# Optimization experiments

Hardware: AMD Instinct MI355X
Metric: run time of the kernel (lower is better)

## Reference

```python
import jax, jax.numpy as jnp
import numpy as np

B, T, H, I, O, R = 64, 1024, 1024, 8, 8, 4
NOISE_STD, ALPHA = 0.05, 0.2


def setup_inputs() -> dict:
    key = jax.random.key(0)
    ks = jax.random.split(key, 6)
    return {
        "x": jax.random.normal(ks[0], (B, T, I), jnp.float32),
        "noise": jax.random.normal(ks[1], (B, T, H), jnp.float32),
        "wi": jax.random.normal(ks[2], (I, H), jnp.float32),
        "si": jnp.ones((I,), jnp.float32),
        "m": jax.random.normal(ks[3], (H, R), jnp.float32),
        "n": jax.random.normal(ks[4], (H, R), jnp.float32),
        "b": jnp.zeros((H,), jnp.float32),
        "wo": jax.random.normal(ks[5], (H, O), jnp.float32) / H,
        "so": jnp.ones((O,), jnp.float32),
        "h0": jnp.zeros((H,), jnp.float32),
    }


def reference(x, noise, wi, si, m, n, b, wo, so, h0):
    hidden = h0.shape[0]
    batch = x.shape[0]
    wi_full = wi * si[:, None]          # (I, H): (wi.T * si).T
    wo_full = wo * so                   # (H, O)
    h_init = jnp.broadcast_to(h0, (batch, hidden))
    r_init = jnp.tanh(h_init)           # non_linearity(initial_states)
    # precompute input drive for all steps: (B,T,H) -> scan over time-major
    u = jnp.einsum('bti,ih->tbh', x, wi_full)
    noise_t = jnp.transpose(noise, (1, 0, 2))  # (T,B,H)

    def step(carry, inp):
        h, r = carry
        u_i, nz_i = inp
        rec = (r @ n) @ m.T / hidden                    # low-rank recurrence
        h = h + NOISE_STD * nz_i + ALPHA * (-h + rec + u_i)
        r = jnp.tanh(h + b)
        out = h @ wo_full                               # identity output nonlin
        return (h, r), out

    _, outs = jax.lax.scan(step, (h_init, r_init), (u, noise_t))
    return jnp.transpose(outs, (1, 0, 2))  # (B,T,O)
```

## Files before the change

### kernel.cpp

```cpp
#include <hip/hip_runtime.h>

#define BB 64
#define TT 1024
#define HH 1024
#define II 8
#define OO 8
#define RRK 4
#define NOISE_STD 0.05f
#define ALPHA 0.2f

typedef float v4f __attribute__((ext_vector_type(4)));
typedef float v2f __attribute__((ext_vector_type(2)));

#define C2E 2.885390081777927f

template<int CTRL, int RM>
__device__ __forceinline__ float dpp_add(float acc, float src) {
    int s = __builtin_amdgcn_update_dpp(0, __float_as_int(src), CTRL, RM, 0xF, true);
    return acc + __int_as_float(s);
}

__device__ __forceinline__ float wave_sum(float x) {
    x = dpp_add<0xB1, 0xF>(x, x);
    x = dpp_add<0x4E, 0xF>(x, x);
    x = dpp_add<0x141, 0xF>(x, x);
    x = dpp_add<0x140, 0xF>(x, x);
    x = dpp_add<0x142, 0xA>(x, x);
    x = dpp_add<0x143, 0xC>(x, x);
    return x;
}

__device__ __forceinline__ float tanh_from_l2x(float l2x) {
    float e = __builtin_amdgcn_exp2f(l2x);
    float r = __builtin_amdgcn_rcpf(e + 1.0f);
    return fmaf(-2.0f, r, 1.0f);
}

__device__ __forceinline__ void block_sync_lds() {
    asm volatile("s_waitcnt lgkmcnt(0)\n\ts_barrier" ::: "memory");
}

__global__ __launch_bounds__(256)
void prew_kernel(const float* __restrict__ noise, const float* __restrict__ wo,
                 const float* __restrict__ so, float* __restrict__ W) {
    __shared__ __align__(16) float red[2][8][4][8];

    const int tid  = threadIdx.x;
    const int wave = tid >> 6;
    const int lane = tid & 63;
    const int e0   = tid << 2;

    float woa[4][OO];
    {
        float so8[OO];
        #pragma unroll
        for (int o = 0; o < OO; ++o) so8[o] = so[o] * NOISE_STD;
        #pragma unroll
        for (int e = 0; e < 4; ++e) {
            const float4 a4 = *(const float4*)(wo + (e0 + e) * OO);
            const float4 b4 = *(const float4*)(wo + (e0 + e) * OO + 4);
            woa[e][0] = a4.x * so8[0]; woa[e][1] = a4.y * so8[1];
            woa[e][2] = a4.z * so8[2]; woa[e][3] = a4.w * so8[3];
            woa[e][4] = b4.x * so8[4]; woa[e][5] = b4.y * so8[5];
            woa[e][6] = b4.z * so8[6]; woa[e][7] = b4.w * so8[7];
        }
    }

    const int row0 = blockIdx.x * 32;
    float4 nz[8], nzn[8];
    #pragma unroll
    for (int j = 0; j < 8; ++j)
        nz[j] = *(const float4*)(noise + (size_t)(row0 + j) * HH + e0);

    #pragma unroll
    for (int ph = 0; ph < 4; ++ph) {
        const int cur   = ph & 1;
        const int rbase = row0 + ph * 8;

        if (ph < 3) {
            #pragma unroll
            for (int j = 0; j < 8; ++j)
                nzn[j] = *(const float4*)(noise + (size_t)(rbase + 8 + j) * HH + e0);
        }

        #pragma unroll
        for (int j = 0; j < 8; ++j) {
            float op[OO];
            #pragma unroll
            for (int o = 0; o < OO; ++o)
                op[o] = fmaf(nz[j].x, woa[0][o], fmaf(nz[j].y, woa[1][o],
                        fmaf(nz[j].z, woa[2][o], nz[j].w * woa[3][o])));
            #pragma unroll
            for (int o = 0; o < OO; ++o) op[o] = wave_sum(op[o]);
            if (lane == 63) {
                *(float4*)&red[cur][j][wave][0] = make_float4(op[0], op[1], op[2], op[3]);
                *(float4*)&red[cur][j][wave][4] = make_float4(op[4], op[5], op[6], op[7]);
            }
        }
        block_sync_lds();
        if (tid < 64) {
            const int j = tid >> 3, o = tid & 7;
            W[(rbase + j) * OO + o] = (red[cur][j][0][o] + red[cur][j][1][o]) +
                                      (red[cur][j][2][o] + red[cur][j][3][o]);
        }
        #pragma unroll
        for (int j = 0; j < 8; ++j) nz[j] = nzn[j];
    }
}

__global__ __launch_bounds__(512, 1)
void rnn_seq_kernel(const float* __restrict__ x, const float* __restrict__ noise,
                    const float* __restrict__ wi, const float* __restrict__ si,
                    const float* __restrict__ mM, const float* __restrict__ nM,
                    const float* __restrict__ bv, const float* __restrict__ wo,
                    const float* __restrict__ so, const float* __restrict__ h0,
                    const float* __restrict__ W, float* __restrict__ out) {
    __shared__ __align__(16) float lds_x[(TT + 1) * II];
    __shared__ __align__(16) float lds_W[TT * OO];
    __shared__ __align__(16) float lds_out[TT * OO];
    __shared__ __align__(16) float red[4][8][4];
    __shared__ __align__(16) float redc[8][104];
    __shared__ float ambx[104];

    const int tid  = threadIdx.x;
    const int b    = blockIdx.x;
    const int wave = tid >> 6;
    const int lane = tid & 63;
    const int e0   = tid << 1;
    const int oc   = tid & 7;

    {
        const float4* sx = (const float4*)(x + (size_t)b * (TT * II));
        const float4* sw = (const float4*)(W + (size_t)b * (TT * OO));
        float4* dx = (float4*)lds_x;
        float4* dw = (float4*)lds_W;
        #pragma unroll
        for (int k = 0; k < 4; ++k) {
            dx[k * 512 + tid] = sx[k * 512 + tid];
            dw[k * 512 + tid] = sw[k * 512 + tid];
        }
        if (tid < 2) dx[2048 + tid] = sx[2046 + tid];
    }

    v2f wiac[II];
    #pragma unroll
    for (int i = 0; i < II; ++i) {
        const float s  = ALPHA * si[i];
        const v2f w = *(const v2f*)(wi + i * HH + e0);
        wiac[i] = s * w;
    }
    v4f nr0, nr1;
    v4f ma0, ma1;
    v2f mac[RRK];
    {
        const float cs = ALPHA / (float)HH;
        ma0 = cs * *(const v4f*)(mM + (size_t)e0 * RRK);
        ma1 = cs * *(const v4f*)(mM + (size_t)(e0 + 1) * RRK);
        nr0 = *(const v4f*)(nM + (size_t)e0 * RRK);
        nr1 = *(const v4f*)(nM + (size_t)(e0 + 1) * RRK);
        mac[0] = (v2f){ma0.x, ma1.x};
        mac[1] = (v2f){ma0.y, ma1.y};
        mac[2] = (v2f){ma0.z, ma1.z};
        mac[3] = (v2f){ma0.w, ma1.w};
    }
    float woa[2][OO];
    {
        #pragma unroll
        for (int e = 0; e < 2; ++e) {
            const float4 a4 = *(const float4*)(wo + (e0 + e) * OO);
            const float4 b4 = *(const float4*)(wo + (e0 + e) * OO + 4);
            woa[e][0] = a4.x * so[0]; woa[e][1] = a4.y * so[1];
            woa[e][2] = a4.z * so[2]; woa[e][3] = a4.w * so[3];
            woa[e][4] = b4.x * so[4]; woa[e][5] = b4.y * so[5];
            woa[e][6] = b4.z * so[6]; woa[e][7] = b4.w * so[7];
        }
    }
    v2f tb2e, h, r;
    {
        const v2f b2 = *(const v2f*)(bv + e0);
        tb2e = C2E * b2;
        h = *(const v2f*)(h0 + e0);
        v2f targ = C2E * h;
        r.x = tanh_from_l2x(targ.x);
        r.y = tanh_from_l2x(targ.y);
    }

    #pragma unroll
    for (int kg = 0; kg < 26; ++kg) {
        float p[4];
        #pragma unroll
        for (int u = 0; u < 4; ++u) {
            const int k = kg * 4 + u;
            float s;
            if (k < 32) {
                const int q = k >> 3, o = k & 7;
                const float m0 = (q == 0) ? ma0.x : (q == 1) ? ma0.y : (q == 2) ? ma0.z : ma0.w;
                const float m1 = (q == 0) ? ma1.x : (q == 1) ? ma1.y : (q == 2) ? ma1.z : ma1.w;
                s = fmaf(m0, woa[0][o], m1 * woa[1][o]);
            } else if (k < 96) {
                const int i = (k - 32) >> 3, o = k & 7;
                s = fmaf(wiac[i].x, woa[0][o], wiac[i].y * woa[1][o]);
            } else {
                const int o = k - 96;
                s = fmaf(h.x, woa[0][o], h.y * woa[1][o]);
            }
            p[u] = wave_sum(s);
        }
        if (lane == 63)
            *(float4*)&redc[wave][kg * 4] = make_float4(p[0], p[1], p[2], p[3]);
    }
    block_sync_lds();
    if (tid < 104)
        ambx[tid] = ((redc[0][tid] + redc[1][tid]) + (redc[2][tid] + redc[3][tid])) +
                    ((redc[4][tid] + redc[5][tid]) + (redc[6][tid] + redc[7][tid]));
    __syncthreads();

    float Amr[RRK], Bxr[II], y;
    #pragma unroll
    for (int q = 0; q < RRK; ++q) Amr[q] = ambx[q * 8 + oc];
    #pragma unroll
    for (int i = 0; i < II; ++i) Bxr[i] = ambx[32 + i * 8 + oc];
    y = ambx[96 + oc];

    const float* nzp = noise + (size_t)b * (TT * HH) + e0;
    v2f nzb[4];
    #pragma unroll
    for (int j = 0; j < 4; ++j) nzb[j] = *(const v2f*)(nzp + j * HH);

    v4f xqc0 = *(const v4f*)&lds_x[0];
    v4f xqc1 = *(const v4f*)&lds_x[4];
    float wqc = lds_W[oc];

    for (int t0 = 0; t0 < TT; t0 += 4) {
        #pragma unroll
        for (int j = 0; j < 4; ++j) {
            const int t = t0 + j;

            const int tn = t + 1;
            const v4f xqn0 = *(const v4f*)&lds_x[tn * II];
            const v4f xqn1 = *(const v4f*)&lds_x[tn * II + 4];
            const float wqn = lds_W[(tn & (TT - 1)) * OO + oc];

            v4f vpv = r.x * nr0;
            vpv += r.y * nr1;
            float vp0 = wave_sum(vpv.x);
            float vp1 = wave_sum(vpv.y);
            float vp2 = wave_sum(vpv.z);
            float vp3 = wave_sum(vpv.w);
            if (lane == 63)
                *(float4*)&red[j][wave][0] = make_float4(vp0, vp1, vp2, vp3);

            float ybase = fmaf(xqc0.x, Bxr[0], wqc);
            ybase = fmaf(xqc0.y, Bxr[1], ybase);
            ybase = fmaf(xqc0.z, Bxr[2], ybase);
            ybase = fmaf(xqc0.w, Bxr[3], ybase);
            ybase = fmaf(xqc1.x, Bxr[4], ybase);
            ybase = fmaf(xqc1.y, Bxr[5], ybase);
            ybase = fmaf(xqc1.z, Bxr[6], ybase);
            ybase = fmaf(xqc1.w, Bxr[7], ybase);

            v2f auv = xqc0.x * wiac[0];
            auv += xqc0.y * wiac[1];
            auv += xqc0.z * wiac[2];
            auv += xqc0.w * wiac[3];
            auv += xqc1.x * wiac[4];
            auv += xqc1.y * wiac[5];
            auv += xqc1.z * wiac[6];
            auv += xqc1.w * wiac[7];

            block_sync_lds();

            v4f vs;
            {
                const v4f s0 = *(const v4f*)&red[j][0][0];
                const v4f s1 = *(const v4f*)&red[j][1][0];
                const v4f s2 = *(const v4f*)&red[j][2][0];
                const v4f s3 = *(const v4f*)&red[j][3][0];
                const v4f s4 = *(const v4f*)&red[j][4][0];
                const v4f s5 = *(const v4f*)&red[j][5][0];
                const v4f s6 = *(const v4f*)&red[j][6][0];
                const v4f s7 = *(const v4f*)&red[j][7][0];
                vs = ((s0 + s1) + (s2 + s3)) + ((s4 + s5) + (s6 + s7));
            }

            v2f acc = auv;
            acc += vs.x * mac[0];
            acc += vs.y * mac[1];
            acc += vs.z * mac[2];
            acc += vs.w * mac[3];
            h = (1.0f - ALPHA) * h + acc;
            h += NOISE_STD * nzb[j];

            {
                float t4 = fmaf(vs.x, Amr[0], ybase);
                t4 = fmaf(vs.y, Amr[1], t4);
                t4 = fmaf(vs.z, Amr[2], t4);
                t4 = fmaf(vs.w, Amr[3], t4);
                y = fmaf(1.0f - ALPHA, y, t4);
                if (tid < OO) lds_out[t * OO + tid] = y;
            }

            nzb[j] = *(const v2f*)(nzp + ((t + 4) & (TT - 1)) * HH);

            {
                v2f targ = C2E * h + tb2e;
                r.x = tanh_from_l2x(targ.x);
                r.y = tanh_from_l2x(targ.y);
            }

            xqc0 = xqn0; xqc1 = xqn1; wqc = wqn;
        }
    }

    __syncthreads();
    {
        float4* dst = (float4*)(out + (size_t)b * (TT * OO));
        const float4* srcv = (const float4*)lds_out;
        #pragma unroll
        for (int k = 0; k < 4; ++k)
            dst[k * 512 + tid] = srcv[k * 512 + tid];
    }
}

extern "C" void kernel_launch(void* const* d_in, const int* in_sizes, int n_in,
                              void* d_out, int out_size, void* d_ws, size_t ws_size,
                              hipStream_t stream) {
    const float* x     = (const float*)d_in[0];
    const float* noise = (const float*)d_in[1];
    const float* wi    = (const float*)d_in[2];
    const float* si    = (const float*)d_in[3];
    const float* mM    = (const float*)d_in[4];
    const float* nM    = (const float*)d_in[5];
    const float* bv    = (const float*)d_in[6];
    const float* wo    = (const float*)d_in[7];
    const float* so    = (const float*)d_in[8];
    const float* h0    = (const float*)d_in[9];
    float* out = (float*)d_out;
    float* W   = (float*)d_ws;

    prew_kernel<<<dim3(2048), dim3(256), 0, stream>>>(noise, wo, so, W);
    rnn_seq_kernel<<<dim3(BB), dim3(512), 0, stream>>>(
        x, noise, wi, si, mM, nM, bv, wo, so, h0, W, out);
}
```

Baseline: 924.8 us.

## Shrink RNN block to two waves and defer output via parallel chunked scan

The sequential RNN kernel now uses 128 threads with 8 hidden units per thread instead of 512 threads with 2. This cuts the cross-wave reduction to two partial sums per step, so each step's barrier involves fewer waves. The per-step output recurrence is removed from the serial loop. Only the rank-4 projection is stored per step, and outputs are rebuilt afterwards with a chunked linear scan (16 chunks of 64 steps, combined using the decay raised to the 64th power). The trade-off is more per-thread work and registers on the serial critical path, and far fewer waves to hide the noise-load latency.

```diff
diff --git a/kernel.cpp b/kernel.cpp
--- a/kernel.cpp
+++ b/kernel.cpp
@@ -10,7 +10,6 @@
 #define ALPHA 0.2f
 
 typedef float v4f __attribute__((ext_vector_type(4)));
-typedef float v2f __attribute__((ext_vector_type(2)));
 
 #define C2E 2.885390081777927f
 
@@ -108,7 +107,7 @@
     }
 }
 
-__global__ __launch_bounds__(512, 1)
+__global__ __launch_bounds__(128, 1)
 void rnn_seq_kernel(const float* __restrict__ x, const float* __restrict__ noise,
                     const float* __restrict__ wi, const float* __restrict__ si,
                     const float* __restrict__ mM, const float* __restrict__ nM,
@@ -116,73 +115,74 @@
                     const float* __restrict__ so, const float* __restrict__ h0,
                     const float* __restrict__ W, float* __restrict__ out) {
     __shared__ __align__(16) float lds_x[(TT + 1) * II];
-    __shared__ __align__(16) float lds_W[TT * OO];
+    __shared__ __align__(16) float lds_v[TT * RRK];
     __shared__ __align__(16) float lds_out[TT * OO];
-    __shared__ __align__(16) float red[4][8][4];
-    __shared__ __align__(16) float redc[8][104];
+    __shared__ __align__(16) float red[4][2][4];
+    __shared__ __align__(16) float redc[2][104];
     __shared__ float ambx[104];
+    __shared__ float chs[16][OO];
 
     const int tid  = threadIdx.x;
     const int b    = blockIdx.x;
     const int wave = tid >> 6;
     const int lane = tid & 63;
-    const int e0   = tid << 1;
+    const int e0   = tid << 3;
     const int oc   = tid & 7;
 
     {
         const float4* sx = (const float4*)(x + (size_t)b * (TT * II));
-        const float4* sw = (const float4*)(W + (size_t)b * (TT * OO));
         float4* dx = (float4*)lds_x;
-        float4* dw = (float4*)lds_W;
-        #pragma unroll
-        for (int k = 0; k < 4; ++k) {
-            dx[k * 512 + tid] = sx[k * 512 + tid];
-            dw[k * 512 + tid] = sw[k * 512 + tid];
-        }
+        #pragma unroll
+        for (int k = 0; k < 16; ++k)
+            dx[k * 128 + tid] = sx[k * 128 + tid];
         if (tid < 2) dx[2048 + tid] = sx[2046 + tid];
     }
 
-    v2f wiac[II];
+    v4f wiaA[II], wiaB[II];
     #pragma unroll
     for (int i = 0; i < II; ++i) {
-        const float s  = ALPHA * si[i];
-        const v2f w = *(const v2f*)(wi + i * HH + e0);
-        wiac[i] = s * w;
-    }
-    v4f nr0, nr1;
-    v4f ma0, ma1;
-    v2f mac[RRK];
+        const float s = ALPHA * si[i];
+        wiaA[i] = s * *(const v4f*)(wi + (size_t)i * HH + e0);
+        wiaB[i] = s * *(const v4f*)(wi + (size_t)i * HH + e0 + 4);
+    }
+    v4f nrv[8];
+    #pragma unroll
+    for (int e = 0; e < 8; ++e)
+        nrv[e] = *(const v4f*)(nM + (size_t)(e0 + e) * RRK);
+    v4f maA[RRK], maB[RRK];
     {
         const float cs = ALPHA / (float)HH;
-        ma0 = cs * *(const v4f*)(mM + (size_t)e0 * RRK);
-        ma1 = cs * *(const v4f*)(mM + (size_t)(e0 + 1) * RRK);
-        nr0 = *(const v4f*)(nM + (size_t)e0 * RRK);
-        nr1 = *(const v4f*)(nM + (size_t)(e0 + 1) * RRK);
-        mac[0] = (v2f){ma0.x, ma1.x};
-        mac[1] = (v2f){ma0.y, ma1.y};
-        mac[2] = (v2f){ma0.z, ma1.z};
-        mac[3] = (v2f){ma0.w, ma1.w};
-    }
-    float woa[2][OO];
-    {
-        #pragma unroll
-        for (int e = 0; e < 2; ++e) {
-            const float4 a4 = *(const float4*)(wo + (e0 + e) * OO);
-            const float4 b4 = *(const float4*)(wo + (e0 + e) * OO + 4);
-            woa[e][0] = a4.x * so[0]; woa[e][1] = a4.y * so[1];
-            woa[e][2] = a4.z * so[2]; woa[e][3] = a4.w * so[3];
-            woa[e][4] = b4.x * so[4]; woa[e][5] = b4.y * so[5];
-            woa[e][6] = b4.z * so[6]; woa[e][7] = b4.w * so[7];
-        }
-    }
-    v2f tb2e, h, r;
-    {
-        const v2f b2 = *(const v2f*)(bv + e0);
-        tb2e = C2E * b2;
-        h = *(const v2f*)(h0 + e0);
-        v2f targ = C2E * h;
-        r.x = tanh_from_l2x(targ.x);
-        r.y = tanh_from_l2x(targ.y);
+        v4f mrow[8];
+        #pragma unroll
+        for (int e = 0; e < 8; ++e)
+            mrow[e] = cs * *(const v4f*)(mM + (size_t)(e0 + e) * RRK);
+        #pragma unroll
+        for (int q = 0; q < RRK; ++q) {
+            maA[q] = (v4f){mrow[0][q], mrow[1][q], mrow[2][q], mrow[3][q]};
+            maB[q] = (v4f){mrow[4][q], mrow[5][q], mrow[6][q], mrow[7][q]};
+        }
+    }
+    float woa[8][OO];
+    #pragma unroll
+    for (int e = 0; e < 8; ++e) {
+        const float4 a4 = *(const float4*)(wo + (size_t)(e0 + e) * OO);
+        const float4 b4 = *(const float4*)(wo + (size_t)(e0 + e) * OO + 4);
+        woa[e][0] = a4.x * so[0]; woa[e][1] = a4.y * so[1];
+        woa[e][2] = a4.z * so[2]; woa[e][3] = a4.w * so[3];
+        woa[e][4] = b4.x * so[4]; woa[e][5] = b4.y * so[5];
+        woa[e][6] = b4.z * so[6]; woa[e][7] = b4.w * so[7];
+    }
+    v4f tbA, tbB, hA, hB, rA, rB;
+    {
+        tbA = C2E * *(const v4f*)(bv + e0);
+        tbB = C2E * *(const v4f*)(bv + e0 + 4);
+        hA = *(const v4f*)(h0 + e0);
+        hB = *(const v4f*)(h0 + e0 + 4);
+        const v4f ta = C2E * hA, tb = C2E * hB;
+        rA.x = tanh_from_l2x(ta.x); rA.y = tanh_from_l2x(ta.y);
+        rA.z = tanh_from_l2x(ta.z); rA.w = tanh_from_l2x(ta.w);
+        rB.x = tanh_from_l2x(tb.x); rB.y = tanh_from_l2x(tb.y);
+        rB.z = tanh_from_l2x(tb.z); rB.w = tanh_from_l2x(tb.w);
     }
 
     #pragma unroll
@@ -194,15 +194,34 @@
             float s;
             if (k < 32) {
                 const int q = k >> 3, o = k & 7;
-                const float m0 = (q == 0) ? ma0.x : (q == 1) ? ma0.y : (q == 2) ? ma0.z : ma0.w;
-                const float m1 = (q == 0) ? ma1.x : (q == 1) ? ma1.y : (q == 2) ? ma1.z : ma1.w;
-                s = fmaf(m0, woa[0][o], m1 * woa[1][o]);
+                s = maA[q].x * woa[0][o];
+                s = fmaf(maA[q].y, woa[1][o], s);
+                s = fmaf(maA[q].z, woa[2][o], s);
+                s = fmaf(maA[q].w, woa[3][o], s);
+                s = fmaf(maB[q].x, woa[4][o], s);
+                s = fmaf(maB[q].y, woa[5][o], s);
+                s = fmaf(maB[q].z, woa[6][o], s);
+                s = fmaf(maB[q].w, woa[7][o], s);
             } else if (k < 96) {
                 const int i = (k - 32) >> 3, o = k & 7;
-                s = fmaf(wiac[i].x, woa[0][o], wiac[i].y * woa[1][o]);
+                s = wiaA[i].x * woa[0][o];
+                s = fmaf(wiaA[i].y, woa[1][o], s);
+                s = fmaf(wiaA[i].z, woa[2][o], s);
+                s = fmaf(wiaA[i].w, woa[3][o], s);
+                s = fmaf(wiaB[i].x, woa[4][o], s);
+                s = fmaf(wiaB[i].y, woa[5][o], s);
+                s = fmaf(wiaB[i].z, woa[6][o], s);
+                s = fmaf(wiaB[i].w, woa[7][o], s);
             } else {
                 const int o = k - 96;
-                s = fmaf(h.x, woa[0][o], h.y * woa[1][o]);
+                s = hA.x * woa[0][o];
+                s = fmaf(hA.y, woa[1][o], s);
+                s = fmaf(hA.z, woa[2][o], s);
+                s = fmaf(hA.w, woa[3][o], s);
+                s = fmaf(hB.x, woa[4][o], s);
+                s = fmaf(hB.y, woa[5][o], s);
+                s = fmaf(hB.z, woa[6][o], s);
+                s = fmaf(hB.w, woa[7][o], s);
             }
             p[u] = wave_sum(s);
         }
@@ -211,114 +230,140 @@
     }
     block_sync_lds();
     if (tid < 104)
-        ambx[tid] = ((redc[0][tid] + redc[1][tid]) + (redc[2][tid] + redc[3][tid])) +
-                    ((redc[4][tid] + redc[5][tid]) + (redc[6][tid] + redc[7][tid]));
+        ambx[tid] = redc[0][tid] + redc[1][tid];
     __syncthreads();
 
-    float Amr[RRK], Bxr[II], y;
+    const float* nzp0 = noise + (size_t)b * (TT * HH) + e0;
+    v4f nzA[4], nzB[4];
+    #pragma unroll
+    for (int j = 0; j < 4; ++j) {
+        nzA[j] = *(const v4f*)(nzp0 + (size_t)j * HH);
+        nzB[j] = *(const v4f*)(nzp0 + (size_t)j * HH + 4);
+    }
+    const float* nzq = nzp0 + (size_t)4 * HH;
+
+    v4f xc0 = *(const v4f*)&lds_x[0];
+    v4f xc1 = *(const v4f*)&lds_x[4];
+
+#define RNN_STEP(t, j, PF)                                                     \
+    {                                                                          \
+        const v4f xn0 = *(const v4f*)&lds_x[((t) + 1) * II];                   \
+        const v4f xn1 = *(const v4f*)&lds_x[((t) + 1) * II + 4];               \
+        v4f vpa = rA.x * nrv[0];                                               \
+        v4f vpb = rB.x * nrv[4];                                               \
+        vpa += rA.y * nrv[1]; vpb += rB.y * nrv[5];                            \
+        vpa += rA.z * nrv[2]; vpb += rB.z * nrv[6];                            \
+        vpa += rA.w * nrv[3]; vpb += rB.w * nrv[7];                            \
+        const v4f vp = vpa + vpb;                                              \
+        const float vp0 = wave_sum(vp.x); const float vp1 = wave_sum(vp.y);    \
+        const float vp2 = wave_sum(vp.z); const float vp3 = wave_sum(vp.w);    \
+        if (lane == 63)                                                        \
+            *(float4*)&red[j][wave][0] = make_float4(vp0, vp1, vp2, vp3);      \
+        v4f auA = xc0.x * wiaA[0], auB = xc0.x * wiaB[0];                      \
+        auA += xc0.y * wiaA[1]; auB += xc0.y * wiaB[1];                        \
+        auA += xc0.z * wiaA[2]; auB += xc0.z * wiaB[2];                        \
+        auA += xc0.w * wiaA[3]; auB += xc0.w * wiaB[3];                        \
+        auA += xc1.x * wiaA[4]; auB += xc1.x * wiaB[4];                        \
+        auA += xc1.y * wiaA[5]; auB += xc1.y * wiaB[5];                        \
+        auA += xc1.z * wiaA[6]; auB += xc1.z * wiaB[6];                        \
+        auA += xc1.w * wiaA[7]; auB += xc1.w * wiaB[7];                        \
+        block_sync_lds();                                                      \
+        const v4f vs = *(const v4f*)&red[j][0][0] + *(const v4f*)&red[j][1][0];\
+        if (tid == 0) *(v4f*)&lds_v[(t) * RRK] = vs;                           \
+        v4f accA = auA + vs.x * maA[0], accB = auB + vs.x * maB[0];            \
+        accA += vs.y * maA[1]; accB += vs.y * maB[1];                          \
+        accA += vs.z * maA[2]; accB += vs.z * maB[2];                          \
+        accA += vs.w * maA[3]; accB += vs.w * maB[3];                          \
+        hA = (1.0f - ALPHA) * hA + accA;  hA += NOISE_STD * nzA[j];            \
+        hB = (1.0f - ALPHA) * hB + accB;  hB += NOISE_STD * nzB[j];            \
+        if (PF) {                                                              \
+            nzA[j] = *(const v4f*)nzq;                                         \
+            nzB[j] = *(const v4f*)(nzq + 4);                                   \
+            nzq += HH;                                                         \
+        }                                                                      \
+        const v4f tgA = C2E * hA + tbA, tgB = C2E * hB + tbB;                  \
+        rA.x = tanh_from_l2x(tgA.x); rA.y = tanh_from_l2x(tgA.y);              \
+        rA.z = tanh_from_l2x(tgA.z); rA.w = tanh_from_l2x(tgA.w);              \
+        rB.x = tanh_from_l2x(tgB.x); rB.y = tanh_from_l2x(tgB.y);              \
+        rB.z = tanh_from_l2x(tgB.z); rB.w = tanh_from_l2x(tgB.w);              \
+        xc0 = xn0; xc1 = xn1;                                                  \
+    }
+
+    for (int t0 = 0; t0 < TT - 4; t0 += 4) {
+        RNN_STEP(t0 + 0, 0, 1)
+        RNN_STEP(t0 + 1, 1, 1)
+        RNN_STEP(t0 + 2, 2, 1)
+        RNN_STEP(t0 + 3, 3, 1)
+    }
+    RNN_STEP(TT - 4, 0, 0)
+    RNN_STEP(TT - 3, 1, 0)
+    RNN_STEP(TT - 2, 2, 0)
+    RNN_STEP(TT - 1, 3, 0)
+#undef RNN_STEP
+
+    __syncthreads();
+
+    float Bxr[II], Amr[RRK];
     #pragma unroll
     for (int q = 0; q < RRK; ++q) Amr[q] = ambx[q * 8 + oc];
     #pragma unroll
     for (int i = 0; i < II; ++i) Bxr[i] = ambx[32 + i * 8 + oc];
-    y = ambx[96 + oc];
-
-    const float* nzp = noise + (size_t)b * (TT * HH) + e0;
-    v2f nzb[4];
-    #pragma unroll
-    for (int j = 0; j < 4; ++j) nzb[j] = *(const v2f*)(nzp + j * HH);
-
-    v4f xqc0 = *(const v4f*)&lds_x[0];
-    v4f xqc1 = *(const v4f*)&lds_x[4];
-    float wqc = lds_W[oc];
-
-    for (int t0 = 0; t0 < TT; t0 += 4) {
-        #pragma unroll
-        for (int j = 0; j < 4; ++j) {
-            const int t = t0 + j;
-
-            const int tn = t + 1;
-            const v4f xqn0 = *(const v4f*)&lds_x[tn * II];
-            const v4f xqn1 = *(const v4f*)&lds_x[tn * II + 4];
-            const float wqn = lds_W[(tn & (TT - 1)) * OO + oc];
-
-            v4f vpv = r.x * nr0;
-            vpv += r.y * nr1;
-            float vp0 = wave_sum(vpv.x);
-            float vp1 = wave_sum(vpv.y);
-            float vp2 = wave_sum(vpv.z);
-            float vp3 = wave_sum(vpv.w);
-            if (lane == 63)
-                *(float4*)&red[j][wave][0] = make_float4(vp0, vp1, vp2, vp3);
-
-            float ybase = fmaf(xqc0.x, Bxr[0], wqc);
-            ybase = fmaf(xqc0.y, Bxr[1], ybase);
-            ybase = fmaf(xqc0.z, Bxr[2], ybase);
-            ybase = fmaf(xqc0.w, Bxr[3], ybase);
-            ybase = fmaf(xqc1.x, Bxr[4], ybase);
-            ybase = fmaf(xqc1.y, Bxr[5], ybase);
-            ybase = fmaf(xqc1.z, Bxr[6], ybase);
-            ybase = fmaf(xqc1.w, Bxr[7], ybase);
-
-            v2f auv = xqc0.x * wiac[0];
-            auv += xqc0.y * wiac[1];
-            auv += xqc0.z * wiac[2];
-            auv += xqc0.w * wiac[3];
-            auv += xqc1.x * wiac[4];
-            auv += xqc1.y * wiac[5];
-            auv += xqc1.z * wiac[6];
-            auv += xqc1.w * wiac[7];
-
-            block_sync_lds();
-
-            v4f vs;
-            {
-                const v4f s0 = *(const v4f*)&red[j][0][0];
-                const v4f s1 = *(const v4f*)&red[j][1][0];
-                const v4f s2 = *(const v4f*)&red[j][2][0];
-                const v4f s3 = *(const v4f*)&red[j][3][0];
-                const v4f s4 = *(const v4f*)&red[j][4][0];
-                const v4f s5 = *(const v4f*)&red[j][5][0];
-                const v4f s6 = *(const v4f*)&red[j][6][0];
-                const v4f s7 = *(const v4f*)&red[j][7][0];
-                vs = ((s0 + s1) + (s2 + s3)) + ((s4 + s5) + (s6 + s7));
-            }
-
-            v2f acc = auv;
-            acc += vs.x * mac[0];
-            acc += vs.y * mac[1];
-            acc += vs.z * mac[2];
-            acc += vs.w * mac[3];
-            h = (1.0f - ALPHA) * h + acc;
-            h += NOISE_STD * nzb[j];
-
-            {
-                float t4 = fmaf(vs.x, Amr[0], ybase);
-                t4 = fmaf(vs.y, Amr[1], t4);
-                t4 = fmaf(vs.z, Amr[2], t4);
-                t4 = fmaf(vs.w, Amr[3], t4);
-                y = fmaf(1.0f - ALPHA, y, t4);
-                if (tid < OO) lds_out[t * OO + tid] = y;
-            }
-
-            nzb[j] = *(const v2f*)(nzp + ((t + 4) & (TT - 1)) * HH);
-
-            {
-                v2f targ = C2E * h + tb2e;
-                r.x = tanh_from_l2x(targ.x);
-                r.y = tanh_from_l2x(targ.y);
-            }
-
-            xqc0 = xqn0; xqc1 = xqn1; wqc = wqn;
-        }
-    }
-
+    const float y0v = ambx[96 + oc];
+
+    const int c   = tid >> 3;
+    const int t0c = c * 64;
+    float a64;
+    {
+        float a = 1.0f - ALPHA;
+        a = a * a; a = a * a; a = a * a;
+        a = a * a; a = a * a; a = a * a;
+        a64 = a;
+    }
+    const float* Wb = W + (size_t)b * (TT * OO);
+    float st[64];
+    float L = 0.0f;
+    #pragma unroll
+    for (int jt = 0; jt < 64; ++jt) {
+        const int t = t0c + jt;
+        const v4f xa = *(const v4f*)&lds_x[t * II];
+        const v4f xb = *(const v4f*)&lds_x[t * II + 4];
+        const v4f vv = *(const v4f*)&lds_v[t * RRK];
+        float s = Wb[t * OO + oc];
+        s = fmaf(xa.x, Bxr[0], s); s = fmaf(xa.y, Bxr[1], s);
+        s = fmaf(xa.z, Bxr[2], s); s = fmaf(xa.w, Bxr[3], s);
+        s = fmaf(xb.x, Bxr[4], s); s = fmaf(xb.y, Bxr[5], s);
+        s = fmaf(xb.z, Bxr[6], s); s = fmaf(xb.w, Bxr[7], s);
+        s = fmaf(vv.x, Amr[0], s); s = fmaf(vv.y, Amr[1], s);
+        s = fmaf(vv.z, Amr[2], s); s = fmaf(vv.w, Amr[3], s);
+        st[jt] = s;
+        L = fmaf(1.0f - ALPHA, L, s);
+    }
+    chs[c][oc] = L;
+    block_sync_lds();
+    if (tid < OO) {
+        float Y = ambx[96 + tid];
+        #pragma unroll
+        for (int c2 = 0; c2 < 16; ++c2) {
+            const float Lc = chs[c2][tid];
+            chs[c2][tid] = Y;
+            Y = fmaf(a64, Y, Lc);
+        }
+    }
+    block_sync_lds();
+    float yv = chs[c][oc];
+    (void)y0v;
+    #pragma unroll
+    for (int jt = 0; jt < 64; ++jt) {
+        yv = fmaf(1.0f - ALPHA, yv, st[jt]);
+        lds_out[(t0c + jt) * OO + oc] = yv;
+    }
     __syncthreads();
     {
         float4* dst = (float4*)(out + (size_t)b * (TT * OO));
         const float4* srcv = (const float4*)lds_out;
         #pragma unroll
-        for (int k = 0; k < 4; ++k)
-            dst[k * 512 + tid] = srcv[k * 512 + tid];
+        for (int k = 0; k < 16; ++k)
+            dst[k * 128 + tid] = srcv[k * 128 + tid];
     }
 }
 
@@ -339,6 +384,6 @@
     float* W   = (float*)d_ws;
 
     prew_kernel<<<dim3(2048), dim3(256), 0, stream>>>(noise, wo, so, W);
-    rnn_seq_kernel<<<dim3(BB), dim3(512), 0, stream>>>(
+    rnn_seq_kernel<<<dim3(BB), dim3(128), 0, stream>>>(
         x, noise, wi, si, mM, nM, bv, wo, so, h0, W, out);
 }
```

After: 864.6 us. -6.5%, faster.

## Run recurrence in a single wave per batch and parallel-scan the output

Applied to the files above, without the earlier changes.

The sequential kernel now uses one 64-lane wave per batch row, with each lane owning 16 hidden units instead of two. This removes the per-step block barrier and the cross-wave LDS reduction, since the rank-4 projection is reduced entirely within the wave using DPP and shuffles. The output recurrence y is moved out of the time loop: the per-step rank values are stored in LDS, and afterwards y is computed as a chunked linear scan over 8 chunks of 128 steps. In exchange each lane carries far more serial work per step, with 16 tanh evaluations and larger register state, and occupancy is limited to one wave per CU.

```diff
diff --git a/kernel.cpp b/kernel.cpp
--- a/kernel.cpp
+++ b/kernel.cpp
@@ -10,7 +10,6 @@
 #define ALPHA 0.2f
 
 typedef float v4f __attribute__((ext_vector_type(4)));
-typedef float v2f __attribute__((ext_vector_type(2)));
 
 #define C2E 2.885390081777927f
 
@@ -30,6 +29,16 @@
     return x;
 }
 
+__device__ __forceinline__ float wave_sum_all(float x) {
+    x = dpp_add<0xB1, 0xF>(x, x);
+    x = dpp_add<0x4E, 0xF>(x, x);
+    x = dpp_add<0x141, 0xF>(x, x);
+    x = dpp_add<0x140, 0xF>(x, x);
+    x += __shfl_xor(x, 16);
+    x += __shfl_xor(x, 32);
+    return x;
+}
+
 __device__ __forceinline__ float tanh_from_l2x(float l2x) {
     float e = __builtin_amdgcn_exp2f(l2x);
     float r = __builtin_amdgcn_rcpf(e + 1.0f);
@@ -38,6 +47,10 @@
 
 __device__ __forceinline__ void block_sync_lds() {
     asm volatile("s_waitcnt lgkmcnt(0)\n\ts_barrier" ::: "memory");
+}
+
+__device__ __forceinline__ void lds_fence() {
+    asm volatile("s_waitcnt lgkmcnt(0)" ::: "memory");
 }
 
 __global__ __launch_bounds__(256)
@@ -108,7 +121,7 @@
     }
 }
 
-__global__ __launch_bounds__(512, 1)
+__global__ __launch_bounds__(64, 1)
 void rnn_seq_kernel(const float* __restrict__ x, const float* __restrict__ noise,
                     const float* __restrict__ wi, const float* __restrict__ si,
                     const float* __restrict__ mM, const float* __restrict__ nM,
@@ -117,17 +130,14 @@
                     const float* __restrict__ W, float* __restrict__ out) {
     __shared__ __align__(16) float lds_x[(TT + 1) * II];
     __shared__ __align__(16) float lds_W[TT * OO];
-    __shared__ __align__(16) float lds_out[TT * OO];
-    __shared__ __align__(16) float red[4][8][4];
-    __shared__ __align__(16) float redc[8][104];
+    __shared__ __align__(16) float lds_v[TT * RRK];
     __shared__ float ambx[104];
-
-    const int tid  = threadIdx.x;
+    __shared__ float chs[8][OO];
+
+    const int lane = threadIdx.x;
     const int b    = blockIdx.x;
-    const int wave = tid >> 6;
-    const int lane = tid & 63;
-    const int e0   = tid << 1;
-    const int oc   = tid & 7;
+    const int e0   = lane << 4;
+    const int oc   = lane & 7;
 
     {
         const float4* sx = (const float4*)(x + (size_t)b * (TT * II));
@@ -135,190 +145,226 @@
         float4* dx = (float4*)lds_x;
         float4* dw = (float4*)lds_W;
         #pragma unroll
-        for (int k = 0; k < 4; ++k) {
-            dx[k * 512 + tid] = sx[k * 512 + tid];
-            dw[k * 512 + tid] = sw[k * 512 + tid];
-        }
-        if (tid < 2) dx[2048 + tid] = sx[2046 + tid];
-    }
-
-    v2f wiac[II];
+        for (int k = 0; k < 32; ++k) {
+            dx[k * 64 + lane] = sx[k * 64 + lane];
+            dw[k * 64 + lane] = sw[k * 64 + lane];
+        }
+        if (lane < 2) dx[2048 + lane] = sx[2046 + lane];
+    }
+
+    v4f wia[II][4];
     #pragma unroll
     for (int i = 0; i < II; ++i) {
-        const float s  = ALPHA * si[i];
-        const v2f w = *(const v2f*)(wi + i * HH + e0);
-        wiac[i] = s * w;
-    }
-    v4f nr0, nr1;
-    v4f ma0, ma1;
-    v2f mac[RRK];
+        const float s = ALPHA * si[i];
+        #pragma unroll
+        for (int g = 0; g < 4; ++g)
+            wia[i][g] = s * *(const v4f*)(wi + (size_t)i * HH + e0 + g * 4);
+    }
+    v4f mag[4][RRK];
     {
         const float cs = ALPHA / (float)HH;
-        ma0 = cs * *(const v4f*)(mM + (size_t)e0 * RRK);
-        ma1 = cs * *(const v4f*)(mM + (size_t)(e0 + 1) * RRK);
-        nr0 = *(const v4f*)(nM + (size_t)e0 * RRK);
-        nr1 = *(const v4f*)(nM + (size_t)(e0 + 1) * RRK);
-        mac[0] = (v2f){ma0.x, ma1.x};
-        mac[1] = (v2f){ma0.y, ma1.y};
-        mac[2] = (v2f){ma0.z, ma1.z};
-        mac[3] = (v2f){ma0.w, ma1.w};
-    }
-    float woa[2][OO];
-    {
-        #pragma unroll
-        for (int e = 0; e < 2; ++e) {
-            const float4 a4 = *(const float4*)(wo + (e0 + e) * OO);
-            const float4 b4 = *(const float4*)(wo + (e0 + e) * OO + 4);
+        v4f mrow[16];
+        #pragma unroll
+        for (int e = 0; e < 16; ++e)
+            mrow[e] = cs * *(const v4f*)(mM + (size_t)(e0 + e) * RRK);
+        #pragma unroll
+        for (int g = 0; g < 4; ++g) {
+            #pragma unroll
+            for (int q = 0; q < RRK; ++q)
+                mag[g][q] = (v4f){mrow[g*4+0][q], mrow[g*4+1][q],
+                                  mrow[g*4+2][q], mrow[g*4+3][q]};
+        }
+    }
+    v4f h[4], r[4], tb[4];
+    #pragma unroll
+    for (int g = 0; g < 4; ++g) {
+        h[g]  = *(const v4f*)(h0 + e0 + g * 4);
+        tb[g] = C2E * *(const v4f*)(bv + e0 + g * 4);
+        const v4f tg = C2E * h[g];
+        r[g].x = tanh_from_l2x(tg.x); r[g].y = tanh_from_l2x(tg.y);
+        r[g].z = tanh_from_l2x(tg.z); r[g].w = tanh_from_l2x(tg.w);
+    }
+
+    {
+        float woa[16][OO];
+        #pragma unroll
+        for (int e = 0; e < 16; ++e) {
+            const float4 a4 = *(const float4*)(wo + (size_t)(e0 + e) * OO);
+            const float4 b4 = *(const float4*)(wo + (size_t)(e0 + e) * OO + 4);
             woa[e][0] = a4.x * so[0]; woa[e][1] = a4.y * so[1];
             woa[e][2] = a4.z * so[2]; woa[e][3] = a4.w * so[3];
             woa[e][4] = b4.x * so[4]; woa[e][5] = b4.y * so[5];
             woa[e][6] = b4.z * so[6]; woa[e][7] = b4.w * so[7];
         }
-    }
-    v2f tb2e, h, r;
-    {
-        const v2f b2 = *(const v2f*)(bv + e0);
-        tb2e = C2E * b2;
-        h = *(const v2f*)(h0 + e0);
-        v2f targ = C2E * h;
-        r.x = tanh_from_l2x(targ.x);
-        r.y = tanh_from_l2x(targ.y);
-    }
-
-    #pragma unroll
-    for (int kg = 0; kg < 26; ++kg) {
-        float p[4];
-        #pragma unroll
-        for (int u = 0; u < 4; ++u) {
-            const int k = kg * 4 + u;
-            float s;
-            if (k < 32) {
-                const int q = k >> 3, o = k & 7;
-                const float m0 = (q == 0) ? ma0.x : (q == 1) ? ma0.y : (q == 2) ? ma0.z : ma0.w;
-                const float m1 = (q == 0) ? ma1.x : (q == 1) ? ma1.y : (q == 2) ? ma1.z : ma1.w;
-                s = fmaf(m0, woa[0][o], m1 * woa[1][o]);
-            } else if (k < 96) {
-                const int i = (k - 32) >> 3, o = k & 7;
-                s = fmaf(wiac[i].x, woa[0][o], wiac[i].y * woa[1][o]);
-            } else {
-                const int o = k - 96;
-                s = fmaf(h.x, woa[0][o], h.y * woa[1][o]);
+        #pragma unroll
+        for (int kg = 0; kg < 26; ++kg) {
+            float p[4];
+            #pragma unroll
+            for (int u = 0; u < 4; ++u) {
+                const int k = kg * 4 + u;
+                float s = 0.0f;
+                if (k < 32) {
+                    const int q = k >> 3, o = k & 7;
+                    #pragma unroll
+                    for (int g = 0; g < 4; ++g) {
+                        s = fmaf(mag[g][q].x, woa[g*4+0][o], s);
+                        s = fmaf(mag[g][q].y, woa[g*4+1][o], s);
+                        s = fmaf(mag[g][q].z, woa[g*4+2][o], s);
+                        s = fmaf(mag[g][q].w, woa[g*4+3][o], s);
+                    }
+                } else if (k < 96) {
+                    const int i = (k - 32) >> 3, o = k & 7;
+                    #pragma unroll
+                    for (int g = 0; g < 4; ++g) {
+                        s = fmaf(wia[i][g].x, woa[g*4+0][o], s);
+                        s = fmaf(wia[i][g].y, woa[g*4+1][o], s);
+                        s = fmaf(wia[i][g].z, woa[g*4+2][o], s);
+                        s = fmaf(wia[i][g].w, woa[g*4+3][o], s);
+                    }
+                } else {
+                    const int o = k - 96;
+                    #pragma unroll
+                    for (int g = 0; g < 4; ++g) {
+                        s = fmaf(h[g].x, woa[g*4+0][o], s);
+                        s = fmaf(h[g].y, woa[g*4+1][o], s);
+                        s = fmaf(h[g].z, woa[g*4+2][o], s);
+                        s = fmaf(h[g].w, woa[g*4+3][o], s);
+                    }
+                }
+                p[u] = wave_sum_all(s);
             }
-            p[u] = wave_sum(s);
-        }
-        if (lane == 63)
-            *(float4*)&redc[wave][kg * 4] = make_float4(p[0], p[1], p[2], p[3]);
-    }
-    block_sync_lds();
-    if (tid < 104)
-        ambx[tid] = ((redc[0][tid] + redc[1][tid]) + (redc[2][tid] + redc[3][tid])) +
-                    ((redc[4][tid] + redc[5][tid]) + (redc[6][tid] + redc[7][tid]));
-    __syncthreads();
-
-    float Amr[RRK], Bxr[II], y;
+            if (lane == 0)
+                *(v4f*)&ambx[kg * 4] = (v4f){p[0], p[1], p[2], p[3]};
+        }
+    }
+    v4f nrv[16];
+    #pragma unroll
+    for (int e = 0; e < 16; ++e)
+        nrv[e] = *(const v4f*)(nM + (size_t)(e0 + e) * RRK);
+
+    lds_fence();
+
+    const float* nzp = noise + (size_t)b * (TT * HH) + e0;
+    v4f nzA[4], nzB[4];
+    #pragma unroll
+    for (int g = 0; g < 4; ++g) {
+        nzA[g] = *(const v4f*)(nzp + g * 4);
+        nzB[g] = *(const v4f*)(nzp + (size_t)HH + g * 4);
+    }
+    v4f xc0 = *(const v4f*)&lds_x[0];
+    v4f xc1 = *(const v4f*)&lds_x[4];
+
+#define RNN_STEP(t, NZ)                                                        \
+    {                                                                          \
+        const v4f xn0 = *(const v4f*)&lds_x[((t) + 1) * II];                   \
+        const v4f xn1 = *(const v4f*)&lds_x[((t) + 1) * II + 4];               \
+                  \
+        v4f c0 = r[0].x * nrv[0];  c0 += r[0].y * nrv[1];                      \
+        c0 += r[0].z * nrv[2];     c0 += r[0].w * nrv[3];                      \
+        v4f c1 = r[1].x * nrv[4];  c1 += r[1].y * nrv[5];                      \
+        c1 += r[1].z * nrv[6];     c1 += r[1].w * nrv[7];                      \
+        v4f c2 = r[2].x * nrv[8];  c2 += r[2].y * nrv[9];                      \
+        c2 += r[2].z * nrv[10];    c2 += r[2].w * nrv[11];                     \
+        v4f c3 = r[3].x * nrv[12]; c3 += r[3].y * nrv[13];                     \
+        c3 += r[3].z * nrv[14];    c3 += r[3].w * nrv[15];                     \
+        const v4f vp = (c0 + c1) + (c2 + c3);                                  \
+        const float v0 = wave_sum_all(vp.x);                                   \
+        const float v1 = wave_sum_all(vp.y);                                   \
+        const float v2 = wave_sum_all(vp.z);                                   \
+        const float v3 = wave_sum_all(vp.w);                                   \
+        if (lane == 0)                                                         \
+            *(v4f*)&lds_v[(t) * RRK] = (v4f){v0, v1, v2, v3};                  \
+                                   \
+        _Pragma("unroll")                                                      \
+        for (int g = 0; g < 4; ++g) {                                          \
+            v4f a = xc0.x * wia[0][g];                                         \
+            a += xc0.y * wia[1][g];  a += xc0.z * wia[2][g];                   \
+            a += xc0.w * wia[3][g];  a += xc1.x * wia[4][g];                   \
+            a += xc1.y * wia[5][g];  a += xc1.z * wia[6][g];                   \
+            a += xc1.w * wia[7][g];                                            \
+            a += v0 * mag[g][0];     a += v1 * mag[g][1];                      \
+            a += v2 * mag[g][2];     a += v3 * mag[g][3];                      \
+            h[g] = (1.0f - ALPHA) * h[g] + a;                                  \
+            h[g] += NOISE_STD * NZ[g];                                         \
+        }                                                                      \
+              \
+        {                                                                      \
+            const int tf = ((t) + 2 < TT) ? (t) + 2 : TT - 1;                  \
+            const float* np = nzp + (size_t)tf * HH;                           \
+            _Pragma("unroll")                                                  \
+            for (int g = 0; g < 4; ++g) NZ[g] = *(const v4f*)(np + g * 4);     \
+        }                                                                      \
+                                                          \
+        _Pragma("unroll")                                                      \
+        for (int g = 0; g < 4; ++g) {                                          \
+            const v4f tg = C2E * h[g] + tb[g];                                 \
+            r[g].x = tanh_from_l2x(tg.x); r[g].y = tanh_from_l2x(tg.y);        \
+            r[g].z = tanh_from_l2x(tg.z); r[g].w = tanh_from_l2x(tg.w);        \
+        }                                                                      \
+        xc0 = xn0; xc1 = xn1;                                                  \
+    }
+
+    for (int t = 0; t < TT; t += 2) {
+        RNN_STEP(t, nzA)
+        RNN_STEP(t + 1, nzB)
+    }
+#undef RNN_STEP
+
+    lds_fence();
+
+    float Amr[RRK], Bxr[II];
     #pragma unroll
     for (int q = 0; q < RRK; ++q) Amr[q] = ambx[q * 8 + oc];
     #pragma unroll
     for (int i = 0; i < II; ++i) Bxr[i] = ambx[32 + i * 8 + oc];
-    y = ambx[96 + oc];
-
-    const float* nzp = noise + (size_t)b * (TT * HH) + e0;
-    v2f nzb[4];
-    #pragma unroll
-    for (int j = 0; j < 4; ++j) nzb[j] = *(const v2f*)(nzp + j * HH);
-
-    v4f xqc0 = *(const v4f*)&lds_x[0];
-    v4f xqc1 = *(const v4f*)&lds_x[4];
-    float wqc = lds_W[oc];
-
-    for (int t0 = 0; t0 < TT; t0 += 4) {
-        #pragma unroll
-        for (int j = 0; j < 4; ++j) {
-            const int t = t0 + j;
-
-            const int tn = t + 1;
-            const v4f xqn0 = *(const v4f*)&lds_x[tn * II];
-            const v4f xqn1 = *(const v4f*)&lds_x[tn * II + 4];
-            const float wqn = lds_W[(tn & (TT - 1)) * OO + oc];
-
-            v4f vpv = r.x * nr0;
-            vpv += r.y * nr1;
-            float vp0 = wave_sum(vpv.x);
-            float vp1 = wave_sum(vpv.y);
-            float vp2 = wave_sum(vpv.z);
-            float vp3 = wave_sum(vpv.w);
-            if (lane == 63)
-                *(float4*)&red[j][wave][0] = make_float4(vp0, vp1, vp2, vp3);
-
-            float ybase = fmaf(xqc0.x, Bxr[0], wqc);
-            ybase = fmaf(xqc0.y, Bxr[1], ybase);
-            ybase = fmaf(xqc0.z, Bxr[2], ybase);
-            ybase = fmaf(xqc0.w, Bxr[3], ybase);
-            ybase = fmaf(xqc1.x, Bxr[4], ybase);
-            ybase = fmaf(xqc1.y, Bxr[5], ybase);
-            ybase = fmaf(xqc1.z, Bxr[6], ybase);
-            ybase = fmaf(xqc1.w, Bxr[7], ybase);
-
-            v2f auv = xqc0.x * wiac[0];
-            auv += xqc0.y * wiac[1];
-            auv += xqc0.z * wiac[2];
-            auv += xqc0.w * wiac[3];
-            auv += xqc1.x * wiac[4];
-            auv += xqc1.y * wiac[5];
-            auv += xqc1.z * wiac[6];
-            auv += xqc1.w * wiac[7];
-
-            block_sync_lds();
-
-            v4f vs;
-            {
-                const v4f s0 = *(const v4f*)&red[j][0][0];
-                const v4f s1 = *(const v4f*)&red[j][1][0];
-                const v4f s2 = *(const v4f*)&red[j][2][0];
-                const v4f s3 = *(const v4f*)&red[j][3][0];
-                const v4f s4 = *(const v4f*)&red[j][4][0];
-                const v4f s5 = *(const v4f*)&red[j][5][0];
-                const v4f s6 = *(const v4f*)&red[j][6][0];
-                const v4f s7 = *(const v4f*)&red[j][7][0];
-                vs = ((s0 + s1) + (s2 + s3)) + ((s4 + s5) + (s6 + s7));
-            }
-
-            v2f acc = auv;
-            acc += vs.x * mac[0];
-            acc += vs.y * mac[1];
-            acc += vs.z * mac[2];
-            acc += vs.w * mac[3];
-            h = (1.0f - ALPHA) * h + acc;
-            h += NOISE_STD * nzb[j];
-
-            {
-                float t4 = fmaf(vs.x, Amr[0], ybase);
-                t4 = fmaf(vs.y, Amr[1], t4);
-                t4 = fmaf(vs.z, Amr[2], t4);
-                t4 = fmaf(vs.w, Amr[3], t4);
-                y = fmaf(1.0f - ALPHA, y, t4);
-                if (tid < OO) lds_out[t * OO + tid] = y;
-            }
-
-            nzb[j] = *(const v2f*)(nzp + ((t + 4) & (TT - 1)) * HH);
-
-            {
-                v2f targ = C2E * h + tb2e;
-                r.x = tanh_from_l2x(targ.x);
-                r.y = tanh_from_l2x(targ.y);
-            }
-
-            xqc0 = xqn0; xqc1 = xqn1; wqc = wqn;
-        }
-    }
-
-    __syncthreads();
-    {
-        float4* dst = (float4*)(out + (size_t)b * (TT * OO));
-        const float4* srcv = (const float4*)lds_out;
-        #pragma unroll
-        for (int k = 0; k < 4; ++k)
-            dst[k * 512 + tid] = srcv[k * 512 + tid];
+
+    const int c   = lane >> 3;
+    const int tc  = c * 128;
+    float a128;
+    {
+        float a = 1.0f - ALPHA;
+        #pragma unroll
+        for (int k = 0; k < 7; ++k) a = a * a;
+        a128 = a;
+    }
+
+    auto step_s = [&](int t) -> float {
+        const v4f xa  = *(const v4f*)&lds_x[t * II];
+        const v4f xb2 = *(const v4f*)&lds_x[t * II + 4];
+        const v4f vv  = *(const v4f*)&lds_v[t * RRK];
+        float s = lds_W[t * OO + oc];
+        s = fmaf(xa.x,  Bxr[0], s); s = fmaf(xa.y,  Bxr[1], s);
+        s = fmaf(xa.z,  Bxr[2], s); s = fmaf(xa.w,  Bxr[3], s);
+        s = fmaf(xb2.x, Bxr[4], s); s = fmaf(xb2.y, Bxr[5], s);
+        s = fmaf(xb2.z, Bxr[6], s); s = fmaf(xb2.w, Bxr[7], s);
+        s = fmaf(vv.x,  Amr[0], s); s = fmaf(vv.y,  Amr[1], s);
+        s = fmaf(vv.z,  Amr[2], s); s = fmaf(vv.w,  Amr[3], s);
+        return s;
+    };
+
+    float L = 0.0f;
+    #pragma unroll 4
+    for (int jt = 0; jt < 128; ++jt)
+        L = fmaf(1.0f - ALPHA, L, step_s(tc + jt));
+    chs[c][oc] = L;
+    lds_fence();
+    if (lane < OO) {
+        float Y = ambx[96 + lane];
+        #pragma unroll
+        for (int c2 = 0; c2 < 8; ++c2) {
+            const float Lc = chs[c2][lane];
+            chs[c2][lane] = Y;
+            Y = fmaf(a128, Y, Lc);
+        }
+    }
+    lds_fence();
+    float yv = chs[c][oc];
+    float* ob = out + (size_t)b * (TT * OO);
+    #pragma unroll 4
+    for (int jt = 0; jt < 128; ++jt) {
+        const int t = tc + jt;
+        yv = fmaf(1.0f - ALPHA, yv, step_s(t));
+        ob[t * OO + oc] = yv;
     }
 }
 
@@ -339,6 +385,6 @@
     float* W   = (float*)d_ws;
 
     prew_kernel<<<dim3(2048), dim3(256), 0, stream>>>(noise, wo, so, W);
-    rnn_seq_kernel<<<dim3(BB), dim3(512), 0, stream>>>(
+    rnn_seq_kernel<<<dim3(BB), dim3(64), 0, stream>>>(
         x, noise, wi, si, mM, nM, bv, wo, so, h0, W, out);
 }
```

New measurement: 1.544 ms. 67.0% more time.
